# Optimization experiments

Hardware: AMD Instinct MI355X
Metric: run time of the kernel (lower is better)

The kernel has to match this reference:

```python
import jax, jax.numpy as jnp
import numpy as np

N_NODES = 50000
N_EDGES = 600000
HIDDEN = 128


def _sage_conv(x, src, dst, W_l, W_r, b):
    """PyG SAGEConv with mean aggregation:
    out_i = W_l @ mean_{j in N(i)} x_j + W_r @ x_i + b
    src/dst: [E] edge endpoints (message flows src -> dst).
    """
    msg = x[src]  # [E, d] gather
    agg = jax.ops.segment_sum(msg, dst, num_segments=N_NODES)  # [N, d]
    cnt = jax.ops.segment_sum(jnp.ones((src.shape[0],), x.dtype), dst,
                              num_segments=N_NODES)  # [N]
    mean = agg / jnp.maximum(cnt, 1.0)[:, None]
    return mean @ W_l.T + x @ W_r.T + b


def setup_inputs() -> dict:
    key = jax.random.key(0)
    ks = jax.random.split(key, 12)
    x = jax.random.normal(ks[0], (N_NODES, HIDDEN), dtype=jnp.float32)
    edge_index = jax.random.randint(ks[1], (2, N_EDGES), 0, N_NODES, dtype=jnp.int64)
    scale = 1.0 / np.sqrt(HIDDEN)
    inp = {"x": x, "edge_index": edge_index}
    for i, layer in enumerate(["1", "2", "3"]):
        inp["Wl" + layer] = jax.random.uniform(ks[2 + 3 * i], (HIDDEN, HIDDEN),
                                               minval=-scale, maxval=scale, dtype=jnp.float32)
        inp["Wr" + layer] = jax.random.uniform(ks[3 + 3 * i], (HIDDEN, HIDDEN),
                                               minval=-scale, maxval=scale, dtype=jnp.float32)
        inp["b" + layer] = jax.random.uniform(ks[4 + 3 * i], (HIDDEN,),
                                              minval=-scale, maxval=scale, dtype=jnp.float32)
    return inp


def reference(x, edge_index, Wl1, Wr1, b1, Wl2, Wr2, b2, Wl3, Wr3, b3):
    src, dst = edge_index[0], edge_index[1]
    h = jax.nn.relu(_sage_conv(x, src, dst, Wl1, Wr1, b1))
    h = _sage_conv(h, src, dst, Wl2, Wr2, b2)
    h = _sage_conv(h, src, dst, Wl3, Wr3, b3)
    return h
```

## Files before the change

### kernel.cpp

```cpp
#include <hip/hip_runtime.h>
#include <hip/hip_bf16.h>

#define N_NODES 50000
#define N_EDGES 600000
#define HID 128

typedef __attribute__((ext_vector_type(8))) short s8v;
typedef __attribute__((ext_vector_type(8))) unsigned short u8v;
typedef __attribute__((ext_vector_type(4))) float f4v;

__device__ __forceinline__ unsigned short f2bf(float x) {
    unsigned u = __float_as_uint(x);
    unsigned r = u + 0x7FFFu + ((u >> 16) & 1u);
    return (unsigned short)(r >> 16);
}
__device__ __forceinline__ float bf2f(unsigned short u) {
    return __uint_as_float((unsigned)u << 16);
}
__device__ __forceinline__ void split_bf(float x, unsigned short& hi, unsigned short& lo) {
    hi = f2bf(x);
    lo = f2bf(x - bf2f(hi));
}

__device__ __forceinline__ int detect_m64(const void* edges) {
    const int* p = (const int*)edges;
    int lane = threadIdx.x & 63;
    unsigned long long nz = __ballot(p[2 * lane + 1] != 0);
    return (nz == 0ULL) ? 1 : 0;
}

__device__ __forceinline__ int edge_at(const void* edges, int mode64, long long idx) {
    return mode64 ? (int)((const long long*)edges)[idx] : ((const int*)edges)[idx];
}

__global__ __launch_bounds__(256) void prep(
    const void* __restrict__ edges, const float* __restrict__ x,
    const float* __restrict__ m0, const float* __restrict__ m1,
    const float* __restrict__ m2, const float* __restrict__ m3,
    const float* __restrict__ m4, const float* __restrict__ m5,
    int* __restrict__ deg,
    unsigned short* __restrict__ whi, unsigned short* __restrict__ wlo,
    unsigned short* __restrict__ xhi, unsigned short* __restrict__ xlo) {
    const int EB  = (N_EDGES + 255) / 256;
    const int WCV = (6 * HID * HID + 255) / 256;
    const int b = blockIdx.x;
    if (b < EB) {
        int m = detect_m64(edges);
        int e = b * 256 + threadIdx.x;
        if (e >= N_EDGES) return;
        int d = edge_at(edges, m, (long long)N_EDGES + e);
        if ((unsigned)d < (unsigned)N_NODES) atomicAdd(&deg[d], 1);
    } else if (b < EB + WCV) {
        int idx = (b - EB) * 256 + threadIdx.x;
        if (idx >= 6 * HID * HID) return;
        int mat = idx >> 14, off = idx & 16383;
        const float* src = mat == 0 ? m0 : mat == 1 ? m1 : mat == 2 ? m2
                         : mat == 3 ? m3 : mat == 4 ? m4 : m5;
        unsigned short h, l;
        split_bf(src[off], h, l);
        whi[idx] = h; wlo[idx] = l;
    } else {
        const int n4 = (N_NODES * HID) / 4;
        int i = (b - EB - WCV) * 256 + threadIdx.x;
        if (i >= n4) return;
        float4 v = ((const float4*)x)[i];
        ushort4 h, l;
        split_bf(v.x, h.x, l.x);
        split_bf(v.y, h.y, l.y);
        split_bf(v.z, h.z, l.z);
        split_bf(v.w, h.w, l.w);
        ((ushort4*)xhi)[i] = h;
        ((ushort4*)xlo)[i] = l;
    }
}

__global__ void scan_block(const int* __restrict__ deg, int* __restrict__ offs,
                           int* __restrict__ blocksum) {
    __shared__ int sm[256];
    int i = blockIdx.x * 256 + threadIdx.x;
    int v = (i < N_NODES) ? deg[i] : 0;
    sm[threadIdx.x] = v;
    __syncthreads();
    #pragma unroll
    for (int s = 1; s < 256; s <<= 1) {
        int t = (threadIdx.x >= (unsigned)s) ? sm[threadIdx.x - s] : 0;
        __syncthreads();
        sm[threadIdx.x] += t;
        __syncthreads();
    }
    if (i < N_NODES) offs[i] = sm[threadIdx.x] - v;
    if (threadIdx.x == 255) blocksum[blockIdx.x] = sm[255];
}

__global__ void scan_top(int* __restrict__ blocksum, int nblocks) {
    __shared__ int sm[256];
    int v = ((int)threadIdx.x < nblocks) ? blocksum[threadIdx.x] : 0;
    sm[threadIdx.x] = v;
    __syncthreads();
    #pragma unroll
    for (int s = 1; s < 256; s <<= 1) {
        int t = (threadIdx.x >= (unsigned)s) ? sm[threadIdx.x - s] : 0;
        __syncthreads();
        sm[threadIdx.x] += t;
        __syncthreads();
    }
    if ((int)threadIdx.x < nblocks) blocksum[threadIdx.x] = sm[threadIdx.x] - v;
    if (threadIdx.x == 255) blocksum[nblocks] = sm[255];
}

__global__ void scan_add(int* __restrict__ offs, int* __restrict__ cursor,
                         const int* __restrict__ blocksum, int nblocks) {
    int i = blockIdx.x * 256 + threadIdx.x;
    if (i < N_NODES) {
        int o = offs[i] + blocksum[blockIdx.x];
        offs[i] = o;
        cursor[i] = o;
    }
    if (i == 0) offs[N_NODES] = blocksum[nblocks];
}

__global__ void fill_csr(const void* __restrict__ edges,
                         int* __restrict__ cursor, int* __restrict__ csr) {
    int m = detect_m64(edges);
    int e = blockIdx.x * 256 + threadIdx.x;
    if (e >= N_EDGES) return;
    int d = edge_at(edges, m, (long long)N_EDGES + e);
    int s = edge_at(edges, m, (long long)e);
    if ((unsigned)d >= (unsigned)N_NODES || (unsigned)s >= (unsigned)N_NODES) return;
    int pos = atomicAdd(&cursor[d], 1);
    csr[pos] = s;
}

template <int RELU, int FINAL>
__global__ __launch_bounds__(256, 2) void sage_fused(
    const unsigned short* __restrict__ Hhi, const unsigned short* __restrict__ Hlo,
    const int* __restrict__ offs, const int* __restrict__ csr,
    const unsigned short* __restrict__ Whi, const unsigned short* __restrict__ Wlo,
    const float* __restrict__ bias,
    unsigned short* __restrict__ ohi, unsigned short* __restrict__ olo,
    float* __restrict__ of32) {
    __shared__ short Mh[64 * 136];
    __shared__ short Ml[64 * 136];
    __shared__ short BhS[128 * 72];
    __shared__ short BlS[128 * 72];

    const int tid = threadIdx.x;
    const int wave = tid >> 6, lane = tid & 63;
    const int mIdx = lane & 15, q = lane >> 4;
    const int wrow = (wave & 1) * 32, wcol = (wave >> 1) * 64;
    const int rowBase = blockIdx.x * 64;

    size_t aoff[2];
    #pragma unroll
    for (int mt = 0; mt < 2; ++mt) {
        int node = rowBase + wrow + mt * 16 + mIdx;
        if (node > N_NODES - 1) node = N_NODES - 1;
        aoff[mt] = (size_t)node * HID + q * 8;
    }
    s8v Hh[2][4], Hl[2][4];
    #pragma unroll
    for (int mt = 0; mt < 2; ++mt)
        #pragma unroll
        for (int c = 0; c < 4; ++c) {
            Hh[mt][c] = *(const s8v*)(Hhi + aoff[mt] + c * 32);
            Hl[mt][c] = *(const s8v*)(Hlo + aoff[mt] + c * 32);
        }

    const int sub = tid & 15;
    const int grp = tid >> 4;
    for (int it = 0; it < 4; ++it) {
        const int r = it * 16 + grp;
        const int node = rowBase + r;
        float a[8] = {0.f, 0.f, 0.f, 0.f, 0.f, 0.f, 0.f, 0.f};
        float inv = 1.0f;
        if (node < N_NODES) {
            const int beg = offs[node], end = offs[node + 1];
            int p = beg;
            for (; p + 8 <= end; p += 8) {
                int s0 = csr[p],     s1 = csr[p + 1], s2 = csr[p + 2], s3 = csr[p + 3];
                int s4 = csr[p + 4], s5 = csr[p + 5], s6 = csr[p + 6], s7 = csr[p + 7];
                u8v v0 = *(const u8v*)(Hhi + (size_t)s0 * HID + sub * 8);
                u8v v1 = *(const u8v*)(Hhi + (size_t)s1 * HID + sub * 8);
                u8v v2 = *(const u8v*)(Hhi + (size_t)s2 * HID + sub * 8);
                u8v v3 = *(const u8v*)(Hhi + (size_t)s3 * HID + sub * 8);
                u8v v4 = *(const u8v*)(Hhi + (size_t)s4 * HID + sub * 8);
                u8v v5 = *(const u8v*)(Hhi + (size_t)s5 * HID + sub * 8);
                u8v v6 = *(const u8v*)(Hhi + (size_t)s6 * HID + sub * 8);
                u8v v7 = *(const u8v*)(Hhi + (size_t)s7 * HID + sub * 8);
                #pragma unroll
                for (int j = 0; j < 8; ++j)
                    a[j] += ((bf2f(v0[j]) + bf2f(v1[j])) + (bf2f(v2[j]) + bf2f(v3[j])))
                          + ((bf2f(v4[j]) + bf2f(v5[j])) + (bf2f(v6[j]) + bf2f(v7[j])));
            }
            if (p + 4 <= end) {
                int s0 = csr[p], s1 = csr[p + 1], s2 = csr[p + 2], s3 = csr[p + 3];
                u8v v0 = *(const u8v*)(Hhi + (size_t)s0 * HID + sub * 8);
                u8v v1 = *(const u8v*)(Hhi + (size_t)s1 * HID + sub * 8);
                u8v v2 = *(const u8v*)(Hhi + (size_t)s2 * HID + sub * 8);
                u8v v3 = *(const u8v*)(Hhi + (size_t)s3 * HID + sub * 8);
                #pragma unroll
                for (int j = 0; j < 8; ++j)
                    a[j] += (bf2f(v0[j]) + bf2f(v1[j])) + (bf2f(v2[j]) + bf2f(v3[j]));
                p += 4;
            }
            for (; p < end; ++p) {
                int s = csr[p];
                u8v v = *(const u8v*)(Hhi + (size_t)s * HID + sub * 8);
                #pragma unroll
                for (int j = 0; j < 8; ++j) a[j] += bf2f(v[j]);
            }
            inv = 1.0f / fmaxf((float)(end - beg), 1.0f);
        }
        u8v hh, ll;
        #pragma unroll
        for (int j = 0; j < 8; ++j) {
            unsigned short hj, lj;
            split_bf(a[j] * inv, hj, lj);
            hh[j] = hj; ll[j] = lj;
        }
        *(u8v*)(Mh + r * 136 + sub * 8) = hh;
        *(u8v*)(Ml + r * 136 + sub * 8) = ll;
    }

    f4v acc[2][4];
    #pragma unroll
    for (int a = 0; a < 2; ++a)
        #pragma unroll
        for (int b = 0; b < 4; ++b) acc[a][b] = (f4v){0.f, 0.f, 0.f, 0.f};

    for (int panel = 0; panel < 4; ++panel) {
        const int ph = panel >> 1;
        const int kb = (panel & 1) * 64;
        const unsigned short* Wh_ = Whi + ph * HID * HID;
        const unsigned short* Wl_ = Wlo + ph * HID * HID;
        __syncthreads();
        {
            const int bcol = tid & 127;
            const int bseg = (tid >> 7) * 32;
            const unsigned short* sh = Wh_ + bcol * HID + kb + bseg;
            const unsigned short* sl = Wl_ + bcol * HID + kb + bseg;
            short* dh = BhS + bcol * 72 + bseg;
            short* dl = BlS + bcol * 72 + bseg;
            #pragma unroll
            for (int j = 0; j < 4; ++j) {
                *(s8v*)(dh + j * 8) = *(const s8v*)(sh + j * 8);
                *(s8v*)(dl + j * 8) = *(const s8v*)(sl + j * 8);
            }
        }
        __syncthreads();
        #pragma unroll
        for (int c = 0; c < 2; ++c) {
            const int kc2 = c * 32;
            s8v Bh_f[4], Bl_f[4];
            #pragma unroll
            for (int nt = 0; nt < 4; ++nt) {
                const int a = (wcol + nt * 16 + mIdx) * 72 + kc2 + q * 8;
                Bh_f[nt] = *(const s8v*)(BhS + a);
                Bl_f[nt] = *(const s8v*)(BlS + a);
            }
            s8v Ah_f[2], Al_f[2];
            if (panel < 2) {
                #pragma unroll
                for (int mt = 0; mt < 2; ++mt) {
                    const int a = (wrow + mt * 16 + mIdx) * 136 + kb + kc2 + q * 8;
                    Ah_f[mt] = *(const s8v*)(Mh + a);
                    Al_f[mt] = *(const s8v*)(Ml + a);
                }
            } else {
                const int idx = (panel - 2) * 2 + c;
                #pragma unroll
                for (int mt = 0; mt < 2; ++mt) {
                    Ah_f[mt] = Hh[mt][idx];
                    Al_f[mt] = Hl[mt][idx];
                }
            }
            #pragma unroll
            for (int mt = 0; mt < 2; ++mt)
                #pragma unroll
                for (int nt = 0; nt < 4; ++nt) {
                    acc[mt][nt] = __builtin_amdgcn_mfma_f32_16x16x32_bf16(
                        Ah_f[mt], Bh_f[nt], acc[mt][nt], 0, 0, 0);
                    acc[mt][nt] = __builtin_amdgcn_mfma_f32_16x16x32_bf16(
                        Al_f[mt], Bh_f[nt], acc[mt][nt], 0, 0, 0);
                    acc[mt][nt] = __builtin_amdgcn_mfma_f32_16x16x32_bf16(
                        Ah_f[mt], Bl_f[nt], acc[mt][nt], 0, 0, 0);
                }
        }
    }

    float bv[4];
    #pragma unroll
    for (int nt = 0; nt < 4; ++nt) bv[nt] = bias[wcol + nt * 16 + mIdx];

    #pragma unroll
    for (int mt = 0; mt < 2; ++mt)
        #pragma unroll
        for (int r = 0; r < 4; ++r) {
            int node = rowBase + wrow + mt * 16 + q * 4 + r;
            if (node < N_NODES) {
                #pragma unroll
                for (int nt = 0; nt < 4; ++nt) {
                    int feat = wcol + nt * 16 + mIdx;
                    float v = acc[mt][nt][r] + bv[nt];
                    if (RELU) v = fmaxf(v, 0.f);
                    size_t oidx = (size_t)node * HID + feat;
                    if (FINAL) {
                        of32[oidx] = v;
                    } else {
                        unsigned short hh, ll;
                        split_bf(v, hh, ll);
                        ohi[oidx] = hh;
                        olo[oidx] = ll;
                    }
                }
            }
        }
}

extern "C" void kernel_launch(void* const* d_in, const int* in_sizes, int n_in,
                              void* d_out, int out_size, void* d_ws, size_t ws_size,
                              hipStream_t stream) {
    const float* x   = (const float*)d_in[0];
    const void* edges = d_in[1];
    const float* Wl1 = (const float*)d_in[2];
    const float* Wr1 = (const float*)d_in[3];
    const float* b1  = (const float*)d_in[4];
    const float* Wl2 = (const float*)d_in[5];
    const float* Wr2 = (const float*)d_in[6];
    const float* b2  = (const float*)d_in[7];
    const float* Wl3 = (const float*)d_in[8];
    const float* Wr3 = (const float*)d_in[9];
    const float* b3  = (const float*)d_in[10];
    float* out = (float*)d_out;

    char* ws = (char*)d_ws;
    size_t off = 0;
    auto alloc = [&](size_t bytes) -> void* {
        void* p = (void*)(ws + off);
        off += (bytes + 255) & ~(size_t)255;
        return p;
    };
    typedef unsigned short u16;
    const size_t FEAT = (size_t)N_NODES * HID;
    int* deg      = (int*)alloc((size_t)N_NODES * 4);
    int* offs     = (int*)alloc((size_t)(N_NODES + 1) * 4);
    int* cursor   = (int*)alloc((size_t)N_NODES * 4);
    int* blocksum = (int*)alloc(256 * 4);
    int* csr      = (int*)alloc((size_t)N_EDGES * 4);
    u16* whi      = (u16*)alloc((size_t)6 * HID * HID * 2);
    u16* wlo      = (u16*)alloc((size_t)6 * HID * HID * 2);
    u16* xhi      = (u16*)alloc(FEAT * 2);
    u16* xlo      = (u16*)alloc(FEAT * 2);
    u16* h1hi     = (u16*)alloc(FEAT * 2);
    u16* h1lo     = (u16*)alloc(FEAT * 2);
    (void)ws_size; (void)in_sizes; (void)n_in; (void)out_size;

    const int EB    = (N_EDGES + 255) / 256;
    const int NB    = (N_NODES + 255) / 256;
    const int WCV   = (6 * HID * HID + 255) / 256;
    const int XSP   = ((int)(FEAT / 4) + 255) / 256;
    const int PREPB = EB + WCV + XSP;
    const int FUSE_B = (N_NODES + 63) / 64;

    hipMemsetAsync(deg, 0, (size_t)N_NODES * 4, stream);
    prep<<<PREPB, 256, 0, stream>>>(edges, x, Wl1, Wr1, Wl2, Wr2, Wl3, Wr3,
                                    deg, whi, wlo, xhi, xlo);
    scan_block<<<NB, 256, 0, stream>>>(deg, offs, blocksum);
    scan_top<<<1, 256, 0, stream>>>(blocksum, NB);
    scan_add<<<NB, 256, 0, stream>>>(offs, cursor, blocksum, NB);
    fill_csr<<<EB, 256, 0, stream>>>(edges, cursor, csr);

    sage_fused<1, 0><<<FUSE_B, 256, 0, stream>>>(xhi, xlo, offs, csr,
        whi, wlo, b1, h1hi, h1lo, (float*)nullptr);
    sage_fused<0, 0><<<FUSE_B, 256, 0, stream>>>(h1hi, h1lo, offs, csr,
        whi + 2 * HID * HID, wlo + 2 * HID * HID, b2, xhi, xlo, (float*)nullptr);
    sage_fused<0, 1><<<FUSE_B, 256, 0, stream>>>(xhi, xlo, offs, csr,
        whi + 4 * HID * HID, wlo + 4 * HID * HID, b3,
        (u16*)nullptr, (u16*)nullptr, out);
}
```

Measured before the change: 369.2 us.

## Halve node tile, read weights directly from global, fold scan_top into scan_add

```diff
diff --git a/kernel.cpp b/kernel.cpp
--- a/kernel.cpp
+++ b/kernel.cpp
@@ -92,31 +92,27 @@
     if (threadIdx.x == 255) blocksum[blockIdx.x] = sm[255];
 }
 
-__global__ void scan_top(int* __restrict__ blocksum, int nblocks) {
-    __shared__ int sm[256];
-    int v = ((int)threadIdx.x < nblocks) ? blocksum[threadIdx.x] : 0;
-    sm[threadIdx.x] = v;
-    __syncthreads();
-    #pragma unroll
-    for (int s = 1; s < 256; s <<= 1) {
-        int t = (threadIdx.x >= (unsigned)s) ? sm[threadIdx.x - s] : 0;
-        __syncthreads();
-        sm[threadIdx.x] += t;
-        __syncthreads();
-    }
-    if ((int)threadIdx.x < nblocks) blocksum[threadIdx.x] = sm[threadIdx.x] - v;
-    if (threadIdx.x == 255) blocksum[nblocks] = sm[255];
-}
-
 __global__ void scan_add(int* __restrict__ offs, int* __restrict__ cursor,
                          const int* __restrict__ blocksum, int nblocks) {
-    int i = blockIdx.x * 256 + threadIdx.x;
+    __shared__ int sm[256];
+    int t = threadIdx.x;
+    int bv = (t < nblocks) ? blocksum[t] : 0;
+    sm[t] = (t < (int)blockIdx.x) ? bv : 0;
+    __syncthreads();
+    #pragma unroll
+    for (int s = 128; s > 0; s >>= 1) {
+        if (t < s) sm[t] += sm[t + s];
+        __syncthreads();
+    }
+    int prefix = sm[0];
+    int i = blockIdx.x * 256 + t;
     if (i < N_NODES) {
-        int o = offs[i] + blocksum[blockIdx.x];
+        int o = offs[i] + prefix;
         offs[i] = o;
         cursor[i] = o;
     }
-    if (i == 0) offs[N_NODES] = blocksum[nblocks];
+    if ((int)blockIdx.x == nblocks - 1 && t == 0)
+        offs[N_NODES] = prefix + blocksum[nblocks - 1];
 }
 
 __global__ void fill_csr(const void* __restrict__ edges,
@@ -132,43 +128,39 @@
 }
 
 template <int RELU, int FINAL>
-__global__ __launch_bounds__(256, 2) void sage_fused(
+__global__ __launch_bounds__(256, 4) void sage_fused(
     const unsigned short* __restrict__ Hhi, const unsigned short* __restrict__ Hlo,
     const int* __restrict__ offs, const int* __restrict__ csr,
     const unsigned short* __restrict__ Whi, const unsigned short* __restrict__ Wlo,
     const float* __restrict__ bias,
     unsigned short* __restrict__ ohi, unsigned short* __restrict__ olo,
     float* __restrict__ of32) {
-    __shared__ short Mh[64 * 136];
-    __shared__ short Ml[64 * 136];
-    __shared__ short BhS[128 * 72];
-    __shared__ short BlS[128 * 72];
+    __shared__ short Mh[32 * 136];
+    __shared__ short Ml[32 * 136];
 
     const int tid = threadIdx.x;
     const int wave = tid >> 6, lane = tid & 63;
     const int mIdx = lane & 15, q = lane >> 4;
-    const int wrow = (wave & 1) * 32, wcol = (wave >> 1) * 64;
-    const int rowBase = blockIdx.x * 64;
-
-    size_t aoff[2];
-    #pragma unroll
-    for (int mt = 0; mt < 2; ++mt) {
-        int node = rowBase + wrow + mt * 16 + mIdx;
+    const int wrow = (wave & 1) * 16, wcol = (wave >> 1) * 64;
+    const int rowBase = blockIdx.x * 32;
+
+    size_t aoff;
+    {
+        int node = rowBase + wrow + mIdx;
         if (node > N_NODES - 1) node = N_NODES - 1;
-        aoff[mt] = (size_t)node * HID + q * 8;
-    }
-    s8v Hh[2][4], Hl[2][4];
-    #pragma unroll
-    for (int mt = 0; mt < 2; ++mt)
-        #pragma unroll
-        for (int c = 0; c < 4; ++c) {
-            Hh[mt][c] = *(const s8v*)(Hhi + aoff[mt] + c * 32);
-            Hl[mt][c] = *(const s8v*)(Hlo + aoff[mt] + c * 32);
-        }
+        aoff = (size_t)node * HID + q * 8;
+    }
+    s8v Hh[4], Hl[4];
+    #pragma unroll
+    for (int c = 0; c < 4; ++c) {
+        Hh[c] = *(const s8v*)(Hhi + aoff + c * 32);
+        Hl[c] = *(const s8v*)(Hlo + aoff + c * 32);
+    }
 
     const int sub = tid & 15;
     const int grp = tid >> 4;
-    for (int it = 0; it < 4; ++it) {
+    #pragma unroll
+    for (int it = 0; it < 2; ++it) {
         const int r = it * 16 + grp;
         const int node = rowBase + r;
         float a[8] = {0.f, 0.f, 0.f, 0.f, 0.f, 0.f, 0.f, 0.f};
@@ -221,100 +213,77 @@
         *(u8v*)(Mh + r * 136 + sub * 8) = hh;
         *(u8v*)(Ml + r * 136 + sub * 8) = ll;
     }
-
-    f4v acc[2][4];
-    #pragma unroll
-    for (int a = 0; a < 2; ++a)
-        #pragma unroll
-        for (int b = 0; b < 4; ++b) acc[a][b] = (f4v){0.f, 0.f, 0.f, 0.f};
-
+    __syncthreads();
+
+    f4v acc[4];
+    #pragma unroll
+    for (int b = 0; b < 4; ++b) acc[b] = (f4v){0.f, 0.f, 0.f, 0.f};
+
+    #pragma unroll
     for (int panel = 0; panel < 4; ++panel) {
         const int ph = panel >> 1;
         const int kb = (panel & 1) * 64;
         const unsigned short* Wh_ = Whi + ph * HID * HID;
         const unsigned short* Wl_ = Wlo + ph * HID * HID;
-        __syncthreads();
-        {
-            const int bcol = tid & 127;
-            const int bseg = (tid >> 7) * 32;
-            const unsigned short* sh = Wh_ + bcol * HID + kb + bseg;
-            const unsigned short* sl = Wl_ + bcol * HID + kb + bseg;
-            short* dh = BhS + bcol * 72 + bseg;
-            short* dl = BlS + bcol * 72 + bseg;
-            #pragma unroll
-            for (int j = 0; j < 4; ++j) {
-                *(s8v*)(dh + j * 8) = *(const s8v*)(sh + j * 8);
-                *(s8v*)(dl + j * 8) = *(const s8v*)(sl + j * 8);
-            }
-        }
-        __syncthreads();
         #pragma unroll
         for (int c = 0; c < 2; ++c) {
-            const int kc2 = c * 32;
+            const int kc = kb + c * 32;
             s8v Bh_f[4], Bl_f[4];
             #pragma unroll
             for (int nt = 0; nt < 4; ++nt) {
-                const int a = (wcol + nt * 16 + mIdx) * 72 + kc2 + q * 8;
-                Bh_f[nt] = *(const s8v*)(BhS + a);
-                Bl_f[nt] = *(const s8v*)(BlS + a);
-            }
-            s8v Ah_f[2], Al_f[2];
+                const size_t wa = (size_t)(wcol + nt * 16 + mIdx) * HID + kc + q * 8;
+                Bh_f[nt] = *(const s8v*)(Wh_ + wa);
+                Bl_f[nt] = *(const s8v*)(Wl_ + wa);
+            }
+            s8v Ah_f, Al_f;
             if (panel < 2) {
-                #pragma unroll
-                for (int mt = 0; mt < 2; ++mt) {
-                    const int a = (wrow + mt * 16 + mIdx) * 136 + kb + kc2 + q * 8;
-                    Ah_f[mt] = *(const s8v*)(Mh + a);
-                    Al_f[mt] = *(const s8v*)(Ml + a);
-                }
+                const int a = (wrow + mIdx) * 136 + kc + q * 8;
+                Ah_f = *(const s8v*)(Mh + a);
+                Al_f = *(const s8v*)(Ml + a);
             } else {
                 const int idx = (panel - 2) * 2 + c;
-                #pragma unroll
-                for (int mt = 0; mt < 2; ++mt) {
-                    Ah_f[mt] = Hh[mt][idx];
-                    Al_f[mt] = Hl[mt][idx];
+                Ah_f = Hh[idx];
+                Al_f = Hl[idx];
+            }
+            __builtin_amdgcn_s_setprio(1);
+            #pragma unroll
+            for (int nt = 0; nt < 4; ++nt) {
+                acc[nt] = __builtin_amdgcn_mfma_f32_16x16x32_bf16(
+                    Ah_f, Bh_f[nt], acc[nt], 0, 0, 0);
+                acc[nt] = __builtin_amdgcn_mfma_f32_16x16x32_bf16(
+                    Al_f, Bh_f[nt], acc[nt], 0, 0, 0);
+                acc[nt] = __builtin_amdgcn_mfma_f32_16x16x32_bf16(
+                    Ah_f, Bl_f[nt], acc[nt], 0, 0, 0);
+            }
+            __builtin_amdgcn_s_setprio(0);
+        }
+    }
+
+    float bv[4];
+    #pragma unroll
+    for (int nt = 0; nt < 4; ++nt) bv[nt] = bias[wcol + nt * 16 + mIdx];
+
+    #pragma unroll
+    for (int r = 0; r < 4; ++r) {
+        int node = rowBase + wrow + q * 4 + r;
+        if (node < N_NODES) {
+            #pragma unroll
+            for (int nt = 0; nt < 4; ++nt) {
+                int feat = wcol + nt * 16 + mIdx;
+                float v = acc[nt][r] + bv[nt];
+                if (RELU) v = fmaxf(v, 0.f);
+                size_t oidx = (size_t)node * HID + feat;
+                if (FINAL) {
+                    of32[oidx] = v;
+                } else {
+                    unsigned short hh, ll;
+                    split_bf(v, hh, ll);
+                    ohi[oidx] = hh;
+                    olo[oidx] = ll;
                 }
             }
-            #pragma unroll
-            for (int mt = 0; mt < 2; ++mt)
-                #pragma unroll
-                for (int nt = 0; nt < 4; ++nt) {
-                    acc[mt][nt] = __builtin_amdgcn_mfma_f32_16x16x32_bf16(
-                        Ah_f[mt], Bh_f[nt], acc[mt][nt], 0, 0, 0);
-                    acc[mt][nt] = __builtin_amdgcn_mfma_f32_16x16x32_bf16(
-                        Al_f[mt], Bh_f[nt], acc[mt][nt], 0, 0, 0);
-                    acc[mt][nt] = __builtin_amdgcn_mfma_f32_16x16x32_bf16(
-                        Ah_f[mt], Bl_f[nt], acc[mt][nt], 0, 0, 0);
-                }
         }
     }
-
-    float bv[4];
-    #pragma unroll
-    for (int nt = 0; nt < 4; ++nt) bv[nt] = bias[wcol + nt * 16 + mIdx];
-
-    #pragma unroll
-    for (int mt = 0; mt < 2; ++mt)
-        #pragma unroll
-        for (int r = 0; r < 4; ++r) {
-            int node = rowBase + wrow + mt * 16 + q * 4 + r;
-            if (node < N_NODES) {
-                #pragma unroll
-                for (int nt = 0; nt < 4; ++nt) {
-                    int feat = wcol + nt * 16 + mIdx;
-                    float v = acc[mt][nt][r] + bv[nt];
-                    if (RELU) v = fmaxf(v, 0.f);
-                    size_t oidx = (size_t)node * HID + feat;
-                    if (FINAL) {
-                        of32[oidx] = v;
-                    } else {
-                        unsigned short hh, ll;
-                        split_bf(v, hh, ll);
-                        ohi[oidx] = hh;
-                        olo[oidx] = ll;
-                    }
-                }
-            }
-        }
 }
 
 extern "C" void kernel_launch(void* const* d_in, const int* in_sizes, int n_in,
@@ -360,13 +329,12 @@
     const int WCV   = (6 * HID * HID + 255) / 256;
     const int XSP   = ((int)(FEAT / 4) + 255) / 256;
     const int PREPB = EB + WCV + XSP;
-    const int FUSE_B = (N_NODES + 63) / 64;
+    const int FUSE_B = (N_NODES + 31) / 32;
 
     hipMemsetAsync(deg, 0, (size_t)N_NODES * 4, stream);
     prep<<<PREPB, 256, 0, stream>>>(edges, x, Wl1, Wr1, Wl2, Wr2, Wl3, Wr3,
                                     deg, whi, wlo, xhi, xlo);
     scan_block<<<NB, 256, 0, stream>>>(deg, offs, blocksum);
-    scan_top<<<1, 256, 0, stream>>>(blocksum, NB);
     scan_add<<<NB, 256, 0, stream>>>(offs, cursor, blocksum, NB);
     fill_csr<<<EB, 256, 0, stream>>>(edges, cursor, csr);
 
```

Measured after the change: 403.0 us. +9.2%, slower.
